# Kernel tuning notes

Hardware: AMD Instinct MI355X
Metric: run time of the kernel (lower is better)

## Reference

```python
import jax, jax.numpy as jnp
import numpy as np

N_NODES = 50000
N_EDGES = 400000
N_GRAPHS = 250
D = 256
NUM_FEATURES = 256
NUM_CLASSES = 10
N_EXTRA_LAYERS = 4  # num_layers - 1
BN_EPS = 1e-5


def _mean_agg(x, src, dst, n):
    # DGL copy_u + mean over incoming edges; zero in-degree nodes get 0.
    s = jax.ops.segment_sum(x[src], dst, num_segments=n)           # [N, d]
    deg = jax.ops.segment_sum(jnp.ones((src.shape[0],), x.dtype), dst, num_segments=n)
    deg = deg[:, None]
    return jnp.where(deg > 0, s / jnp.maximum(deg, 1.0), 0.0)


def _gin_layer(x, src, dst, W1, b1, W2, b2, gamma, beta):
    n = x.shape[0]
    h = x + _mean_agg(x, src, dst, n)                              # (1+eps)*x + agg, eps=0
    h = jax.nn.relu(h @ W1 + b1) @ W2 + b2                         # apply_func MLP
    h = jax.nn.relu(h)                                             # GINConv activation
    mu = h.mean(axis=0)
    var = h.var(axis=0)                                            # biased var (torch BN train)
    return gamma * (h - mu) / jnp.sqrt(var + BN_EPS) + beta


def setup_inputs() -> dict:
    key = jax.random.key(0)
    ks = jax.random.split(key, 24)
    sc_in = 1.0 / np.sqrt(NUM_FEATURES)
    sc = 1.0 / np.sqrt(D)
    inp = {
        "x": jax.random.normal(ks[0], (N_NODES, NUM_FEATURES), dtype=jnp.float32),
        "src": jax.random.randint(ks[1], (N_EDGES,), 0, N_NODES, dtype=jnp.int32),
        "dst": jax.random.randint(ks[2], (N_EDGES,), 0, N_NODES, dtype=jnp.int32),
        "node_counts": jnp.full((N_GRAPHS,), N_NODES // N_GRAPHS, dtype=jnp.int32),
        # conv1 MLP + BN1
        "W1a": jax.random.normal(ks[3], (NUM_FEATURES, D), dtype=jnp.float32) * sc_in,
        "b1a": jnp.zeros((D,), jnp.float32),
        "W1b": jax.random.normal(ks[4], (D, D), dtype=jnp.float32) * sc,
        "b1b": jnp.zeros((D,), jnp.float32),
        "g1": jnp.ones((D,), jnp.float32),
        "be1": jnp.zeros((D,), jnp.float32),
        # stacked convs 2..5 + BNs
        "Ws1": jax.random.normal(ks[5], (N_EXTRA_LAYERS, D, D), dtype=jnp.float32) * sc,
        "bs1": jnp.zeros((N_EXTRA_LAYERS, D), jnp.float32),
        "Ws2": jax.random.normal(ks[6], (N_EXTRA_LAYERS, D, D), dtype=jnp.float32) * sc,
        "bs2": jnp.zeros((N_EXTRA_LAYERS, D), jnp.float32),
        "gammas": jnp.ones((N_EXTRA_LAYERS, D), jnp.float32),
        "betas": jnp.zeros((N_EXTRA_LAYERS, D), jnp.float32),
        # classifier
        "fcW1": jax.random.normal(ks[7], (D, D), dtype=jnp.float32) * sc,
        "fcb1": jnp.zeros((D,), jnp.float32),
        "fcW2": jax.random.normal(ks[8], (D, NUM_CLASSES), dtype=jnp.float32) * sc,
        "fcb2": jnp.zeros((NUM_CLASSES,), jnp.float32),
    }
    return inp


def reference(x, src, dst, node_counts, W1a, b1a, W1b, b1b, g1, be1,
              Ws1, bs1, Ws2, bs2, gammas, betas, fcW1, fcb1, fcW2, fcb2):
    h = _gin_layer(x, src, dst, W1a, b1a, W1b, b1b, g1, be1)
    for i in range(N_EXTRA_LAYERS):
        h = _gin_layer(h, src, dst, Ws1[i], bs1[i], Ws2[i], bs2[i], gammas[i], betas[i])
    # per-graph last-node readout
    last_idx = jnp.cumsum(node_counts) - 1                          # [n_graphs]
    g = h[last_idx]                                                 # [n_graphs, d]
    # dropout is identity in eval mode
    g = jax.nn.relu(g @ fcW1 + fcb1)
    logits = g @ fcW2 + fcb2
    return jax.nn.log_softmax(logits, axis=-1)
```

## Files before the change

### kernel.cpp

```cpp
#include <hip/hip_runtime.h>
#include <hip/hip_bf16.h>

#define N_NODESC 50000
#define N_EDGESC 400000
#define N_GRAPHSC 250
#define DDIM 256
#define NCLS 10
#define BN_EPSF 1e-5f
#define MPAD 50048
#define NBLK_SCAN 196

typedef __attribute__((ext_vector_type(4))) float f32x4;
typedef __attribute__((ext_vector_type(8))) short bf16x8;
typedef __attribute__((ext_vector_type(8))) unsigned short u16x8;

__device__ __forceinline__ float bf2f(unsigned short h) {
    union { unsigned int u; float f; } c;
    c.u = ((unsigned int)h) << 16;
    return c.f;
}
__device__ __forceinline__ unsigned short f2bf(float f) {
    union { float f; unsigned int u; } c;
    c.f = f;
    unsigned int u = c.u;
    return (unsigned short)((u + 0x7FFFu + ((u >> 16) & 1u)) >> 16);
}


__global__ void k_zero32(int* __restrict__ p, int n) {
    int i = blockIdx.x * blockDim.x + threadIdx.x;
    if (i < n) p[i] = 0;
}

__global__ void k_count(const int* __restrict__ dst, int* __restrict__ cnt) {
    int e = blockIdx.x * blockDim.x + threadIdx.x;
    if (e < N_EDGESC) atomicAdd(&cnt[dst[e]], 1);
}

__global__ __launch_bounds__(256) void k_scan1(const int* __restrict__ deg,
                                               int* __restrict__ rowstart,
                                               int* __restrict__ bsum) {
    __shared__ int sh[256];
    int tid = threadIdx.x;
    int i = blockIdx.x * 256 + tid;
    int v = (i < N_NODESC) ? deg[i] : 0;
    sh[tid] = v;
    __syncthreads();
    for (int off = 1; off < 256; off <<= 1) {
        int t = (tid >= off) ? sh[tid - off] : 0;
        __syncthreads();
        sh[tid] += t;
        __syncthreads();
    }
    if (i < N_NODESC) rowstart[i] = sh[tid] - v;
    if (tid == 255) bsum[blockIdx.x] = sh[255];
}

__global__ __launch_bounds__(256) void k_scan2(int* __restrict__ rowstart,
                                               const int* __restrict__ bsum) {
    __shared__ int sh[256];
    int tid = threadIdx.x;
    sh[tid] = (tid < NBLK_SCAN) ? bsum[tid] : 0;
    __syncthreads();
    for (int off = 1; off < 256; off <<= 1) {
        int t = (tid >= off) ? sh[tid - off] : 0;
        __syncthreads();
        sh[tid] += t;
        __syncthreads();
    }
    int i = blockIdx.x * 256 + tid;
    if (blockIdx.x > 0 && i < N_NODESC) rowstart[i] += sh[blockIdx.x - 1];
    if (i == 0) rowstart[N_NODESC] = N_EDGESC;
}

__global__ void k_fill(const int* __restrict__ src, const int* __restrict__ dst,
                       const int* __restrict__ rowstart, int* __restrict__ cur,
                       int* __restrict__ esrc) {
    int e = blockIdx.x * blockDim.x + threadIdx.x;
    if (e < N_EDGESC) {
        int d = dst[e];
        int pos = rowstart[d] + atomicAdd(&cur[d], 1);
        esrc[pos] = src[e];
    }
}


__global__ __launch_bounds__(256) void k_wprep(const float* __restrict__ W1a,
                                               const float* __restrict__ W1b,
                                               const float* __restrict__ Ws1,
                                               const float* __restrict__ Ws2,
                                               unsigned short* __restrict__ Wt) {
    int i = blockIdx.x * blockDim.x + threadIdx.x;
    if (i >= 10 * 65536) return;
    int m = i >> 16;
    int r = i & 65535;
    int n = r >> 8;
    int k = r & 255;
    int l = m >> 1, wsel = m & 1;
    const float* src = (l == 0) ? (wsel ? W1b : W1a)
                                : (wsel ? Ws2 + (size_t)(l - 1) * 65536
                                        : Ws1 + (size_t)(l - 1) * 65536);
    Wt[i] = f2bf(src[(size_t)k * 256 + n]);
}

__global__ __launch_bounds__(256) void k_xbf(const float* __restrict__ X,
                                             unsigned short* __restrict__ Y) {
    int i = blockIdx.x * 256 + threadIdx.x;
    if (i < N_NODESC * 64) {
        float4 v = ((const float4*)X)[i];
        ushort4 o;
        o.x = f2bf(v.x); o.y = f2bf(v.y); o.z = f2bf(v.z); o.w = f2bf(v.w);
        ((ushort4*)Y)[i] = o;
    }
}

__global__ __launch_bounds__(256) void k_agg_bf(const unsigned short* __restrict__ X,
                                                const int* __restrict__ esrc,
                                                const int* __restrict__ rowstart,
                                                const float* __restrict__ stat,
                                                const float* __restrict__ gamma,
                                                const float* __restrict__ beta,
                                                unsigned short* __restrict__ Hout) {
    int node = blockIdx.x * 4 + (threadIdx.x >> 6);
    if (node >= N_NODESC) return;
    int lane = threadIdx.x & 63;
    int d0 = lane * 4;
    float sc[4], tt[4];
    if (stat) {
        const float invN = 1.0f / (float)N_NODESC;
#pragma unroll
        for (int q = 0; q < 4; q++) {
            float mu = stat[d0 + q] * invN;
            float var = stat[256 + d0 + q] * invN - mu * mu;
            float s = gamma[d0 + q] * rsqrtf(var + BN_EPSF);
            sc[q] = s;
            tt[q] = beta[d0 + q] - s * mu;
        }
    } else {
#pragma unroll
        for (int q = 0; q < 4; q++) { sc[q] = 1.f; tt[q] = 0.f; }
    }
    int beg = rowstart[node];
    int end = rowstart[node + 1];
    float a0 = 0.f, a1 = 0.f, a2 = 0.f, a3 = 0.f;
    float b0 = 0.f, b1 = 0.f, b2 = 0.f, b3 = 0.f;
    float c0 = 0.f, c1 = 0.f, c2 = 0.f, c3 = 0.f;
    float e0 = 0.f, e1 = 0.f, e2 = 0.f, e3 = 0.f;
    int j = beg;
    for (; j + 4 <= end; j += 4) {
        int sn0 = esrc[j], sn1 = esrc[j + 1], sn2 = esrc[j + 2], sn3 = esrc[j + 3];
        ushort4 v0 = *(const ushort4*)(X + (size_t)sn0 * DDIM + d0);
        ushort4 v1 = *(const ushort4*)(X + (size_t)sn1 * DDIM + d0);
        ushort4 v2 = *(const ushort4*)(X + (size_t)sn2 * DDIM + d0);
        ushort4 v3 = *(const ushort4*)(X + (size_t)sn3 * DDIM + d0);
        a0 += bf2f(v0.x); a1 += bf2f(v0.y); a2 += bf2f(v0.z); a3 += bf2f(v0.w);
        b0 += bf2f(v1.x); b1 += bf2f(v1.y); b2 += bf2f(v1.z); b3 += bf2f(v1.w);
        c0 += bf2f(v2.x); c1 += bf2f(v2.y); c2 += bf2f(v2.z); c3 += bf2f(v2.w);
        e0 += bf2f(v3.x); e1 += bf2f(v3.y); e2 += bf2f(v3.z); e3 += bf2f(v3.w);
    }
    for (; j < end; j++) {
        int sn0 = esrc[j];
        ushort4 v0 = *(const ushort4*)(X + (size_t)sn0 * DDIM + d0);
        a0 += bf2f(v0.x); a1 += bf2f(v0.y); a2 += bf2f(v0.z); a3 += bf2f(v0.w);
    }
    a0 += b0 + c0 + e0; a1 += b1 + c1 + e1; a2 += b2 + c2 + e2; a3 += b3 + c3 + e3;
    float inv = (end > beg) ? 1.0f / (float)(end - beg) : 0.0f;
    float cnt = (end > beg) ? 2.0f : 1.0f;
    ushort4 xv = *(const ushort4*)(X + (size_t)node * DDIM + d0);
    ushort4 o;
    o.x = f2bf(sc[0] * (bf2f(xv.x) + a0 * inv) + tt[0] * cnt);
    o.y = f2bf(sc[1] * (bf2f(xv.y) + a1 * inv) + tt[1] * cnt);
    o.z = f2bf(sc[2] * (bf2f(xv.z) + a2 * inv) + tt[2] * cnt);
    o.w = f2bf(sc[3] * (bf2f(xv.w) + a3 * inv) + tt[3] * cnt);
    *(ushort4*)(Hout + (size_t)node * DDIM + d0) = o;
}


__global__ __launch_bounds__(512) void k_mlp(const unsigned short* __restrict__ A,
                                             const unsigned short* __restrict__ W1t,
                                             const float* __restrict__ b1,
                                             const unsigned short* __restrict__ W2t,
                                             const float* __restrict__ b2,
                                             unsigned short* __restrict__ C,
                                             float* __restrict__ stat) {
    __shared__ unsigned short Tl[128 * 256];

    const int tid = threadIdx.x;
    const int wv = tid >> 6;
    const int lane = tid & 63;
    const int bm = blockIdx.x;
    const int wr = (wv >> 2) * 64;
    const int wc = (wv & 3) * 64;
    const int lr = lane & 15;
    const int lk = lane >> 4;

    f32x4 acc[4][4];
    bf16x8 bcur[4], bnxt[4];

#pragma unroll
    for (int m = 0; m < 4; m++)
#pragma unroll
        for (int n = 0; n < 4; n++) acc[m][n] = (f32x4)(0.f);

#pragma unroll
    for (int n = 0; n < 4; n++)
        bcur[n] = *(const bf16x8*)(W1t + (size_t)(wc + n * 16 + lr) * 256 + lk * 8);

    for (int k0 = 0; k0 < 256; k0 += 32) {
        bf16x8 af[4];
#pragma unroll
        for (int m = 0; m < 4; m++)
            af[m] = *(const bf16x8*)(A + (size_t)(bm * 128 + wr + m * 16 + lr) * 256 +
                                     k0 + lk * 8);
        if (k0 < 224) {
#pragma unroll
            for (int n = 0; n < 4; n++)
                bnxt[n] = *(const bf16x8*)(W1t + (size_t)(wc + n * 16 + lr) * 256 +
                                           k0 + 32 + lk * 8);
        }
#pragma unroll
        for (int m = 0; m < 4; m++)
#pragma unroll
            for (int n = 0; n < 4; n++)
                acc[m][n] = __builtin_amdgcn_mfma_f32_16x16x32_bf16(af[m], bcur[n],
                                                                    acc[m][n], 0, 0, 0);
#pragma unroll
        for (int n = 0; n < 4; n++) bcur[n] = bnxt[n];
    }
#pragma unroll
    for (int n = 0; n < 4; n++) {
        int col = wc + n * 16 + lr;
        float bv = b1[col];
#pragma unroll
        for (int m = 0; m < 4; m++)
#pragma unroll
            for (int i = 0; i < 4; i++) {
                int row = wr + m * 16 + lk * 4 + i;
                float v = fmaxf(acc[m][n][i] + bv, 0.f);
                Tl[row * 256 + ((col >> 3) ^ (row & 7)) * 8 + (col & 7)] = f2bf(v);
            }
    }
    __syncthreads();

#pragma unroll
    for (int m = 0; m < 4; m++)
#pragma unroll
        for (int n = 0; n < 4; n++) acc[m][n] = (f32x4)(0.f);

#pragma unroll
    for (int n = 0; n < 4; n++)
        bcur[n] = *(const bf16x8*)(W2t + (size_t)(wc + n * 16 + lr) * 256 + lk * 8);

    for (int k0 = 0; k0 < 256; k0 += 32) {
        bf16x8 af[4];
#pragma unroll
        for (int m = 0; m < 4; m++) {
            int row = wr + m * 16 + lr;
            af[m] = ((const bf16x8*)Tl)[row * 32 + (((k0 >> 3) + lk) ^ (row & 7))];
        }
        if (k0 < 224) {
#pragma unroll
            for (int n = 0; n < 4; n++)
                bnxt[n] = *(const bf16x8*)(W2t + (size_t)(wc + n * 16 + lr) * 256 +
                                           k0 + 32 + lk * 8);
        }
#pragma unroll
        for (int m = 0; m < 4; m++)
#pragma unroll
            for (int n = 0; n < 4; n++)
                acc[m][n] = __builtin_amdgcn_mfma_f32_16x16x32_bf16(af[m], bcur[n],
                                                                    acc[m][n], 0, 0, 0);
#pragma unroll
        for (int n = 0; n < 4; n++) bcur[n] = bnxt[n];
    }
    __syncthreads();

#pragma unroll
    for (int n = 0; n < 4; n++) {
        int col = wc + n * 16 + lr;
        float bv = b2[col];
        float sp = 0.f, ssp = 0.f;
#pragma unroll
        for (int m = 0; m < 4; m++)
#pragma unroll
            for (int i = 0; i < 4; i++) {
                int row = wr + m * 16 + lk * 4 + i;
                float v = fmaxf(acc[m][n][i] + bv, 0.f);
                Tl[row * 256 + ((col >> 3) ^ (row & 7)) * 8 + (col & 7)] = f2bf(v);
                if (bm * 128 + row < N_NODESC) { sp += v; ssp += v * v; }
            }
        sp += __shfl_xor(sp, 16);
        sp += __shfl_xor(sp, 32);
        ssp += __shfl_xor(ssp, 16);
        ssp += __shfl_xor(ssp, 32);
        if (lane < 16) {
            atomicAdd(&stat[col], sp);
            atomicAdd(&stat[256 + col], ssp);
        }
    }
    __syncthreads();

#pragma unroll
    for (int it = 0; it < 8; it++) {
        int chunk = it * 512 + tid;
        int row = chunk >> 5;
        int cc = chunk & 31;
        u16x8 v = *(const u16x8*)&Tl[row * 256 + (cc ^ (row & 7)) * 8];
        *(u16x8*)(C + (size_t)(bm * 128 + row) * DDIM + cc * 8) = v;
    }
}


__global__ __launch_bounds__(256) void k_head(const unsigned short* __restrict__ Y,
                                              const int* __restrict__ counts,
                                              const float* __restrict__ stat,
                                              const float* __restrict__ gamma,
                                              const float* __restrict__ beta,
                                              const float* __restrict__ fcW1,
                                              const float* __restrict__ fcb1,
                                              const float* __restrict__ fcW2,
                                              const float* __restrict__ fcb2,
                                              float* __restrict__ out) {
    int g = blockIdx.x;
    __shared__ float row[DDIM];
    __shared__ float gv[DDIM];
    __shared__ float logits[NCLS];
    __shared__ int lastIdx;
    if (threadIdx.x == 0) {
        int s = 0;
        for (int i = 0; i <= g; i++) s += counts[i];
        lastIdx = s - 1;
    }
    __syncthreads();
    int j = threadIdx.x;
    const float invN = 1.0f / (float)N_NODESC;
    float mu = stat[j] * invN;
    float var = stat[256 + j] * invN - mu * mu;
    float sc = gamma[j] * rsqrtf(var + BN_EPSF);
    row[j] = sc * (bf2f(Y[(size_t)lastIdx * DDIM + j]) - mu) + beta[j];
    __syncthreads();
    float acc = fcb1[j];
    for (int d = 0; d < DDIM; d++) acc += row[d] * fcW1[(size_t)d * DDIM + j];
    gv[j] = fmaxf(acc, 0.f);
    __syncthreads();
    if (j < NCLS) {
        float a = fcb2[j];
        for (int d = 0; d < DDIM; d++) a += gv[d] * fcW2[(size_t)d * NCLS + j];
        logits[j] = a;
    }
    __syncthreads();
    if (j == 0) {
        float m = -1e30f;
        for (int c = 0; c < NCLS; c++) m = fmaxf(m, logits[c]);
        float se = 0.f;
        for (int c = 0; c < NCLS; c++) se += expf(logits[c] - m);
        float lse = m + logf(se);
        for (int c = 0; c < NCLS; c++) out[g * NCLS + c] = logits[c] - lse;
    }
}


extern "C" void kernel_launch(void* const* d_in, const int* in_sizes, int n_in,
                              void* d_out, int out_size, void* d_ws, size_t ws_size,
                              hipStream_t stream) {
    const float* x    = (const float*)d_in[0];
    const int* src    = (const int*)d_in[1];
    const int* dst    = (const int*)d_in[2];
    const int* counts = (const int*)d_in[3];
    const float* W1a  = (const float*)d_in[4];
    const float* b1a  = (const float*)d_in[5];
    const float* W1b  = (const float*)d_in[6];
    const float* b1b  = (const float*)d_in[7];
    const float* g1   = (const float*)d_in[8];
    const float* be1  = (const float*)d_in[9];
    const float* Ws1  = (const float*)d_in[10];
    const float* bs1  = (const float*)d_in[11];
    const float* Ws2  = (const float*)d_in[12];
    const float* bs2  = (const float*)d_in[13];
    const float* gms  = (const float*)d_in[14];
    const float* bts  = (const float*)d_in[15];
    const float* fcW1 = (const float*)d_in[16];
    const float* fcb1 = (const float*)d_in[17];
    const float* fcW2 = (const float*)d_in[18];
    const float* fcb2 = (const float*)d_in[19];
    float* out = (float*)d_out;

    char* ws = (char*)d_ws;
    const size_t BUF = (size_t)MPAD * DDIM * 2;
    unsigned short* B0 = (unsigned short*)(ws);
    unsigned short* B1 = (unsigned short*)(ws + BUF);
    unsigned short* Bx = (unsigned short*)(ws + 2 * BUF);
    unsigned short* Wt = (unsigned short*)(ws + 3 * BUF);
    int* rowstart      = (int*)(ws + 3 * BUF + 1310720);
    int* cursor        = (int*)(ws + 3 * BUF + 1510784);
    int* esrc          = (int*)(ws + 3 * BUF + 1710848);
    float* stats       = (float*)(ws + 3 * BUF + 3310848);
    int* bsum          = (int*)(ws + 3 * BUF + 3321088);

    k_zero32<<<dim3((N_NODESC + 255) / 256), 256, 0, stream>>>(cursor, N_NODESC);
    k_count<<<dim3((N_EDGESC + 255) / 256), 256, 0, stream>>>(dst, cursor);
    k_scan1<<<dim3(NBLK_SCAN), 256, 0, stream>>>(cursor, rowstart, bsum);
    k_scan2<<<dim3(NBLK_SCAN), 256, 0, stream>>>(rowstart, bsum);
    k_zero32<<<dim3((N_NODESC + 255) / 256), 256, 0, stream>>>(cursor, N_NODESC);
    k_fill<<<dim3((N_EDGESC + 255) / 256), 256, 0, stream>>>(src, dst, rowstart,
                                                             cursor, esrc);

    k_wprep<<<dim3((10 * 65536 + 255) / 256), 256, 0, stream>>>(W1a, W1b, Ws1, Ws2, Wt);
    k_xbf<<<dim3(12500), 256, 0, stream>>>(x, Bx);
    k_zero32<<<dim3(10), 256, 0, stream>>>((int*)stats, 2560);

    for (int l = 0; l < 5; ++l) {
        const float* B1b = (l == 0) ? b1a : bs1 + (l - 1) * 256;
        const float* B2b = (l == 0) ? b1b : bs2 + (l - 1) * 256;
        const unsigned short* Wt1 = Wt + (size_t)(l * 2) * 65536;
        const unsigned short* Wt2 = Wt + (size_t)(l * 2 + 1) * 65536;

        if (l == 0) {
            k_agg_bf<<<dim3(12500), 256, 0, stream>>>(Bx, esrc, rowstart, nullptr,
                                                      nullptr, nullptr, B1);
        } else {
            const float* GA = (l == 1) ? g1 : gms + (l - 2) * 256;
            const float* BE = (l == 1) ? be1 : bts + (l - 2) * 256;
            k_agg_bf<<<dim3(12500), 256, 0, stream>>>(B0, esrc, rowstart,
                                                      stats + (size_t)(l - 1) * 512,
                                                      GA, BE, B1);
        }
        k_mlp<<<dim3(MPAD / 128), 512, 0, stream>>>(B1, Wt1, B1b, Wt2, B2b, B0,
                                                    stats + (size_t)l * 512);
    }

    k_head<<<dim3(N_GRAPHSC), 256, 0, stream>>>(B0, counts, stats + 4 * 512,
                                                gms + 3 * 256, bts + 3 * 256,
                                                fcW1, fcb1, fcW2, fcb2, out);
}
```

Measured before the change: 636.4 us.

## Shrink MLP tile to 64 rows and replace stat atomics with two-stage reduction

The fused MLP kernel now processes 64-row tiles using 1024 threads, with 16 waves each computing a 16x64 output slice. This doubles the block count and cuts per-wave accumulators, while the next A fragment is prefetched from global memory. BatchNorm statistics are no longer accumulated with global atomics. Each block writes per-block partial sums into a spare workspace region, and two small kernels reduce them deterministically. The smaller tile means less reuse of the weight fragments each wave loads, and each layer now pays two extra launches.

```diff
diff --git a/kernel.cpp b/kernel.cpp
--- a/kernel.cpp
+++ b/kernel.cpp
@@ -8,6 +8,7 @@
 #define NCLS 10
 #define BN_EPSF 1e-5f
 #define MPAD 50048
+#define NBLK_MLP (MPAD / 64)
 #define NBLK_SCAN 196
 
 typedef __attribute__((ext_vector_type(4))) float f32x4;
@@ -113,6 +114,7 @@
         ((ushort4*)Y)[i] = o;
     }
 }
+
 
 __global__ __launch_bounds__(256) void k_agg_bf(const unsigned short* __restrict__ X,
                                                 const int* __restrict__ esrc,
@@ -176,102 +178,90 @@
 }
 
 
-__global__ __launch_bounds__(512) void k_mlp(const unsigned short* __restrict__ A,
-                                             const unsigned short* __restrict__ W1t,
-                                             const float* __restrict__ b1,
-                                             const unsigned short* __restrict__ W2t,
-                                             const float* __restrict__ b2,
-                                             unsigned short* __restrict__ C,
-                                             float* __restrict__ stat) {
-    __shared__ unsigned short Tl[128 * 256];
+__global__ __launch_bounds__(1024) void k_mlp(const unsigned short* __restrict__ A,
+                                              const unsigned short* __restrict__ W1t,
+                                              const float* __restrict__ b1,
+                                              const unsigned short* __restrict__ W2t,
+                                              const float* __restrict__ b2,
+                                              unsigned short* __restrict__ C,
+                                              float* __restrict__ part) {
+    __shared__ unsigned short Tl[64 * 256];
+    __shared__ float sred[4][512];
 
     const int tid = threadIdx.x;
     const int wv = tid >> 6;
     const int lane = tid & 63;
     const int bm = blockIdx.x;
-    const int wr = (wv >> 2) * 64;
+    const int wm = wv >> 2;
     const int wc = (wv & 3) * 64;
     const int lr = lane & 15;
     const int lk = lane >> 4;
 
-    f32x4 acc[4][4];
-    bf16x8 bcur[4], bnxt[4];
-
-#pragma unroll
-    for (int m = 0; m < 4; m++)
-#pragma unroll
-        for (int n = 0; n < 4; n++) acc[m][n] = (f32x4)(0.f);
-
+    f32x4 acc[4];
+
+#pragma unroll
+    for (int n = 0; n < 4; n++) acc[n] = (f32x4)(0.f);
+
+    const unsigned short* Arow = A + (size_t)(bm * 64 + wm * 16 + lr) * 256;
+    bf16x8 a_cur = *(const bf16x8*)(Arow + lk * 8);
+    bf16x8 w_cur[4], w_nxt[4];
 #pragma unroll
     for (int n = 0; n < 4; n++)
-        bcur[n] = *(const bf16x8*)(W1t + (size_t)(wc + n * 16 + lr) * 256 + lk * 8);
-
+        w_cur[n] = *(const bf16x8*)(W1t + (size_t)(wc + n * 16 + lr) * 256 + lk * 8);
+
+#pragma unroll
     for (int k0 = 0; k0 < 256; k0 += 32) {
-        bf16x8 af[4];
-#pragma unroll
-        for (int m = 0; m < 4; m++)
-            af[m] = *(const bf16x8*)(A + (size_t)(bm * 128 + wr + m * 16 + lr) * 256 +
-                                     k0 + lk * 8);
+        bf16x8 a_nxt = a_cur;
         if (k0 < 224) {
+            a_nxt = *(const bf16x8*)(Arow + k0 + 32 + lk * 8);
 #pragma unroll
             for (int n = 0; n < 4; n++)
-                bnxt[n] = *(const bf16x8*)(W1t + (size_t)(wc + n * 16 + lr) * 256 +
-                                           k0 + 32 + lk * 8);
-        }
-#pragma unroll
-        for (int m = 0; m < 4; m++)
-#pragma unroll
-            for (int n = 0; n < 4; n++)
-                acc[m][n] = __builtin_amdgcn_mfma_f32_16x16x32_bf16(af[m], bcur[n],
-                                                                    acc[m][n], 0, 0, 0);
-#pragma unroll
-        for (int n = 0; n < 4; n++) bcur[n] = bnxt[n];
+                w_nxt[n] = *(const bf16x8*)(W1t + (size_t)(wc + n * 16 + lr) * 256 +
+                                            k0 + 32 + lk * 8);
+        }
+#pragma unroll
+        for (int n = 0; n < 4; n++)
+            acc[n] = __builtin_amdgcn_mfma_f32_16x16x32_bf16(a_cur, w_cur[n],
+                                                             acc[n], 0, 0, 0);
+        a_cur = a_nxt;
+#pragma unroll
+        for (int n = 0; n < 4; n++) w_cur[n] = w_nxt[n];
     }
 #pragma unroll
     for (int n = 0; n < 4; n++) {
         int col = wc + n * 16 + lr;
         float bv = b1[col];
 #pragma unroll
-        for (int m = 0; m < 4; m++)
-#pragma unroll
-            for (int i = 0; i < 4; i++) {
-                int row = wr + m * 16 + lk * 4 + i;
-                float v = fmaxf(acc[m][n][i] + bv, 0.f);
-                Tl[row * 256 + ((col >> 3) ^ (row & 7)) * 8 + (col & 7)] = f2bf(v);
-            }
-    }
-    __syncthreads();
-
-#pragma unroll
-    for (int m = 0; m < 4; m++)
-#pragma unroll
-        for (int n = 0; n < 4; n++) acc[m][n] = (f32x4)(0.f);
-
+        for (int i = 0; i < 4; i++) {
+            int row = wm * 16 + lk * 4 + i;
+            float v = fmaxf(acc[n][i] + bv, 0.f);
+            Tl[row * 256 + ((col >> 3) ^ (row & 7)) * 8 + (col & 7)] = f2bf(v);
+        }
+    }
+    __syncthreads();
+
+#pragma unroll
+    for (int n = 0; n < 4; n++) acc[n] = (f32x4)(0.f);
 #pragma unroll
     for (int n = 0; n < 4; n++)
-        bcur[n] = *(const bf16x8*)(W2t + (size_t)(wc + n * 16 + lr) * 256 + lk * 8);
-
+        w_cur[n] = *(const bf16x8*)(W2t + (size_t)(wc + n * 16 + lr) * 256 + lk * 8);
+
+    const int trow = wm * 16 + lr;
+#pragma unroll
     for (int k0 = 0; k0 < 256; k0 += 32) {
-        bf16x8 af[4];
-#pragma unroll
-        for (int m = 0; m < 4; m++) {
-            int row = wr + m * 16 + lr;
-            af[m] = ((const bf16x8*)Tl)[row * 32 + (((k0 >> 3) + lk) ^ (row & 7))];
-        }
+        bf16x8 af = ((const bf16x8*)Tl)[trow * 32 + (((k0 >> 3) + lk) ^ (trow & 7))];
         if (k0 < 224) {
 #pragma unroll
             for (int n = 0; n < 4; n++)
-                bnxt[n] = *(const bf16x8*)(W2t + (size_t)(wc + n * 16 + lr) * 256 +
-                                           k0 + 32 + lk * 8);
-        }
-#pragma unroll
-        for (int m = 0; m < 4; m++)
-#pragma unroll
-            for (int n = 0; n < 4; n++)
-                acc[m][n] = __builtin_amdgcn_mfma_f32_16x16x32_bf16(af[m], bcur[n],
-                                                                    acc[m][n], 0, 0, 0);
-#pragma unroll
-        for (int n = 0; n < 4; n++) bcur[n] = bnxt[n];
+                w_nxt[n] = *(const bf16x8*)(W2t + (size_t)(wc + n * 16 + lr) * 256 +
+                                            k0 + 32 + lk * 8);
+        }
+#pragma unroll
+        for (int n = 0; n < 4; n++)
+            acc[n] = __builtin_amdgcn_mfma_f32_16x16x32_bf16(af, w_cur[n],
+                                                             acc[n], 0, 0, 0);
+#pragma unroll
+        for (int n = 0; n < 4; n++) w_cur[n] = w_nxt[n];
     }
     __syncthreads();
 
@@ -281,33 +271,54 @@
         float bv = b2[col];
         float sp = 0.f, ssp = 0.f;
 #pragma unroll
-        for (int m = 0; m < 4; m++)
-#pragma unroll
-            for (int i = 0; i < 4; i++) {
-                int row = wr + m * 16 + lk * 4 + i;
-                float v = fmaxf(acc[m][n][i] + bv, 0.f);
-                Tl[row * 256 + ((col >> 3) ^ (row & 7)) * 8 + (col & 7)] = f2bf(v);
-                if (bm * 128 + row < N_NODESC) { sp += v; ssp += v * v; }
-            }
+        for (int i = 0; i < 4; i++) {
+            int row = wm * 16 + lk * 4 + i;
+            float v = fmaxf(acc[n][i] + bv, 0.f);
+            Tl[row * 256 + ((col >> 3) ^ (row & 7)) * 8 + (col & 7)] = f2bf(v);
+            if (bm * 64 + row < N_NODESC) { sp += v; ssp += v * v; }
+        }
         sp += __shfl_xor(sp, 16);
         sp += __shfl_xor(sp, 32);
         ssp += __shfl_xor(ssp, 16);
         ssp += __shfl_xor(ssp, 32);
         if (lane < 16) {
-            atomicAdd(&stat[col], sp);
-            atomicAdd(&stat[256 + col], ssp);
-        }
-    }
-    __syncthreads();
-
-#pragma unroll
-    for (int it = 0; it < 8; it++) {
-        int chunk = it * 512 + tid;
+            sred[wm][col] = sp;
+            sred[wm][256 + col] = ssp;
+        }
+    }
+    __syncthreads();
+
+#pragma unroll
+    for (int it = 0; it < 2; it++) {
+        int chunk = it * 1024 + tid;
         int row = chunk >> 5;
         int cc = chunk & 31;
         u16x8 v = *(const u16x8*)&Tl[row * 256 + (cc ^ (row & 7)) * 8];
-        *(u16x8*)(C + (size_t)(bm * 128 + row) * DDIM + cc * 8) = v;
-    }
+        *(u16x8*)(C + (size_t)(bm * 64 + row) * DDIM + cc * 8) = v;
+    }
+    if (tid < 512)
+        part[(size_t)bm * 512 + tid] =
+            sred[0][tid] + sred[1][tid] + sred[2][tid] + sred[3][tid];
+}
+
+
+__global__ __launch_bounds__(512) void k_statred1(const float* __restrict__ part,
+                                                  float* __restrict__ part2) {
+    int t = threadIdx.x;
+    int b0 = blockIdx.x * 23;
+    float s = 0.f;
+#pragma unroll 4
+    for (int j = 0; j < 23; j++) s += part[(size_t)(b0 + j) * 512 + t];
+    part2[(size_t)blockIdx.x * 512 + t] = s;
+}
+
+__global__ __launch_bounds__(512) void k_statred2(const float* __restrict__ part2,
+                                                  float* __restrict__ stat) {
+    int t = threadIdx.x;
+    float s = 0.f;
+#pragma unroll 4
+    for (int j = 0; j < 34; j++) s += part2[(size_t)j * 512 + t];
+    stat[t] = s;
 }
 
 
@@ -390,6 +401,8 @@
     unsigned short* B0 = (unsigned short*)(ws);
     unsigned short* B1 = (unsigned short*)(ws + BUF);
     unsigned short* Bx = (unsigned short*)(ws + 2 * BUF);
+    float* stats_part  = (float*)(ws + 2 * BUF);
+    float* stats_part2 = (float*)(ws + 2 * BUF + 1601536);
     unsigned short* Wt = (unsigned short*)(ws + 3 * BUF);
     int* rowstart      = (int*)(ws + 3 * BUF + 1310720);
     int* cursor        = (int*)(ws + 3 * BUF + 1510784);
@@ -407,7 +420,6 @@
 
     k_wprep<<<dim3((10 * 65536 + 255) / 256), 256, 0, stream>>>(W1a, W1b, Ws1, Ws2, Wt);
     k_xbf<<<dim3(12500), 256, 0, stream>>>(x, Bx);
-    k_zero32<<<dim3(10), 256, 0, stream>>>((int*)stats, 2560);
 
     for (int l = 0; l < 5; ++l) {
         const float* B1b = (l == 0) ? b1a : bs1 + (l - 1) * 256;
@@ -425,8 +437,11 @@
                                                       stats + (size_t)(l - 1) * 512,
                                                       GA, BE, B1);
         }
-        k_mlp<<<dim3(MPAD / 128), 512, 0, stream>>>(B1, Wt1, B1b, Wt2, B2b, B0,
-                                                    stats + (size_t)l * 512);
+        k_mlp<<<dim3(NBLK_MLP), 1024, 0, stream>>>(B1, Wt1, B1b, Wt2, B2b, B0,
+                                                   stats_part);
+        k_statred1<<<dim3(34), 512, 0, stream>>>(stats_part, stats_part2);
+        k_statred2<<<dim3(1), 512, 0, stream>>>(stats_part2,
+                                                stats + (size_t)l * 512);
     }
 
     k_head<<<dim3(N_GRAPHSC), 256, 0, stream>>>(B0, counts, stats + 4 * 512,
```

Result: slower. 1.015 ms (+59.5%).
